# Performance work log

Hardware: AMD Instinct MI355X
Metric: run time of the kernel (lower is better)

The kernel has to match this reference:

```python
import jax, jax.numpy as jnp
import numpy as np
from jax import lax

B, F_BINS, T = 4, 196, 1000
DM, H, DEPTH, FFN, L, EDIM = 512, 8, 64, 2048, 4, 128


def setup_inputs() -> dict:
    key = jax.random.key(0)
    ks = jax.random.split(key, 16)
    d = {}
    d['spec'] = jax.random.normal(ks[0], (B, 1, F_BINS, T), jnp.float32)
    d['conv1_w'] = jax.random.normal(ks[1], (32, 1, 5, 5), jnp.float32) / 5.0
    d['conv1_b'] = jax.random.normal(ks[2], (32,), jnp.float32) * 0.01
    d['conv2_w'] = jax.random.normal(ks[3], (64, 32, 5, 5), jnp.float32) / np.sqrt(32 * 25)
    d['conv2_b'] = jax.random.normal(ks[4], (64,), jnp.float32) * 0.01
    d['proj_w'] = jax.random.normal(ks[5], (DM, 64), jnp.float32) / 8.0
    d['proj_b'] = jnp.zeros((DM,), jnp.float32)
    d['ln1_g'] = jnp.ones((L, DM), jnp.float32)
    d['ln1_b'] = jnp.zeros((L, DM), jnp.float32)
    s = 1.0 / np.sqrt(DM)
    for i, nm in enumerate(['qw', 'kw', 'vw', 'dw']):
        d[nm] = jax.random.normal(ks[6 + i], (L, DM, DM), jnp.float32) * s
    for nm in ['qb', 'kb', 'vb', 'db']:
        d[nm] = jnp.zeros((L, DM), jnp.float32)
    d['Er'] = jax.random.normal(ks[10], (L, T, DEPTH), jnp.float32)
    d['ln2_g'] = jnp.ones((L, DM), jnp.float32)
    d['ln2_b'] = jnp.zeros((L, DM), jnp.float32)
    d['f1w'] = jax.random.normal(ks[11], (L, FFN, DM), jnp.float32) * s
    d['f1b'] = jnp.zeros((L, FFN), jnp.float32)
    d['f2w'] = jax.random.normal(ks[12], (L, DM, FFN), jnp.float32) / np.sqrt(FFN)
    d['f2b'] = jnp.zeros((L, DM), jnp.float32)
    d['deproj_w'] = jax.random.normal(ks[13], (EDIM, DM), jnp.float32) * s
    d['deproj_b'] = jnp.zeros((EDIM,), jnp.float32)
    return d


def _layernorm(x, g, b, eps=1e-5):
    mu = jnp.mean(x, -1, keepdims=True)
    var = jnp.mean(jnp.square(x - mu), -1, keepdims=True)
    return g * (x - mu) / jnp.sqrt(var + eps) + b


def _skew(QEr):
    # QEr: [B,H,S,S] -> music-transformer skew trick
    b, h, s, _ = QEr.shape
    padded = jnp.pad(QEr, ((0, 0), (0, 0), (0, 0), (1, 0)))  # [B,H,S,S+1]
    return padded.reshape(b, h, s + 1, s)[:, :, 1:, :]


def _forward(spec, conv1_w, conv1_b, conv2_w, conv2_b, proj_w, proj_b,
             ln1_g, ln1_b, qw, qb, kw, kb, vw, vb, dw, db, Er,
             ln2_g, ln2_b, f1w, f1b, f2w, f2b, deproj_w, deproj_b):
    dn = ('NCHW', 'OIHW', 'NCHW')
    x = lax.conv_general_dilated(spec, conv1_w, (1, 1), 'SAME', dimension_numbers=dn)
    x = jax.nn.gelu(x + conv1_b[None, :, None, None], approximate=False)
    x = lax.reduce_window(x, -jnp.inf, lax.max, (1, 1, 14, 1), (1, 1, 14, 1), 'VALID')
    x = lax.conv_general_dilated(x, conv2_w, (1, 1), 'SAME', dimension_numbers=dn)
    x = jax.nn.gelu(x + conv2_b[None, :, None, None], approximate=False)
    x = lax.reduce_window(x, -jnp.inf, lax.max, (1, 1, 14, 1), (1, 1, 14, 1), 'VALID')
    x = x.reshape(B, 64, T)              # freq collapsed to 1, flatten(1,2)
    x = x.transpose(0, 2, 1)             # [B,T,64]
    x = x @ proj_w.T + proj_b            # [B,T,DM]
    scale = 1.0 / np.sqrt(DEPTH)
    for l in range(L):
        xn = _layernorm(x, ln1_g[l], ln1_b[l])
        Q = (xn @ qw[l].T + qb[l]).reshape(B, T, H, DEPTH).transpose(0, 2, 1, 3)
        K = (xn @ kw[l].T + kb[l]).reshape(B, T, H, DEPTH).transpose(0, 2, 1, 3)
        V = (xn @ vw[l].T + vb[l]).reshape(B, T, H, DEPTH).transpose(0, 2, 1, 3)
        QEr = jnp.einsum('bhsd,rd->bhsr', Q, Er[l])        # relative pos scores
        Srel = _skew(QEr)
        logits = (jnp.einsum('bhsd,bhtd->bhst', Q, K) + Srel) * scale
        attn = jax.nn.softmax(logits, axis=-1)
        out = jnp.einsum('bhst,bhtd->bhsd', attn, V)
        out = out.transpose(0, 2, 1, 3).reshape(B, T, DM)
        x = x + (out @ dw[l].T + db[l])
        xn2 = _layernorm(x, ln2_g[l], ln2_b[l])
        ff = jax.nn.relu(xn2 @ f1w[l].T + f1b[l]) @ f2w[l].T + f2b[l]
        x = x + ff
    return x @ deproj_w.T + deproj_b     # [B,T,EDIM]


def reference(spec, conv1_w, conv1_b, conv2_w, conv2_b, proj_w, proj_b,
              ln1_g, ln1_b, qw, qb, kw, kb, vw, vb, dw, db, Er,
              ln2_g, ln2_b, f1w, f1b, f2w, f2b, deproj_w, deproj_b):
    return _forward(spec, conv1_w, conv1_b, conv2_w, conv2_b, proj_w, proj_b,
                    ln1_g, ln1_b, qw, qb, kw, kb, vw, vb, dw, db, Er,
                    ln2_g, ln2_b, f1w, f1b, f2w, f2b, deproj_w, deproj_b)
```

## Files before the change

### kernel.cpp

```cpp
#include <hip/hip_runtime.h>
#include <hip/hip_bf16.h>
#include <hip/hip_fp16.h>
#include <math.h>

#define BB 4
#define FBINS 196
#define TT 1000
#define DM 512
#define HH 8
#define DEPTH 64
#define FFN 2048
#define LL 4
#define EDIM 128
#define BT (BB*TT)
#define PSHIFT 12.0f

typedef __hip_bfloat16 bf16;
typedef __attribute__((ext_vector_type(8))) short short8;
typedef __attribute__((ext_vector_type(4))) float floatx4;

#define ARENA_BYTES 420000000ULL
static void* g_arena = nullptr;
__attribute__((constructor)) static void arena_init() {
    if (!g_arena) (void)hipMalloc(&g_arena, ARENA_BYTES);
}

__device__ __forceinline__ float gelu_f(float x) {
    return 0.5f * x * (1.0f + erff(x * 0.70710678118654752440f));
}

__global__ __launch_bounds__(256) void sniff_k(const unsigned short* __restrict__ p,
                                               int n, int* __restrict__ cnt) {
    int i = blockIdx.x * 256 + threadIdx.x;
    int c = 0;
    for (; i < n; i += gridDim.x * 256) {
        unsigned short u = p[i];
        if ((unsigned short)(u & 0x7FFF) > (unsigned short)0x7F80) c++;
    }
    if (c) atomicAdd(cnt, c);
}

#define NCVT 17
struct CvtArgs {
    const void* src[NCVT];
    unsigned dst[NCVT];
    unsigned cum[NCVT + 1];
    const int* cnt;
    float* dstA;
};
__global__ __launch_bounds__(256) void cvt_all(CvtArgs a) {
    unsigned i = blockIdx.x * 256 + threadIdx.x;
    if (i >= a.cum[NCVT]) return;
    bool isb = (*a.cnt == 0);
    int w = 0;
    while (i >= a.cum[w + 1]) w++;
    unsigned j = i - a.cum[w];
    float v = isb ? __bfloat162float(((const bf16*)a.src[w])[j])
                  : ((const float*)a.src[w])[j];
    a.dstA[a.dst[w] + j] = v;
}

__global__ __launch_bounds__(256) void f2bf_dyn(const void* __restrict__ src,
                                                bf16* __restrict__ d, int n,
                                                const int* __restrict__ cnt) {
    int i = blockIdx.x * 256 + threadIdx.x;
    if (i >= n) return;
    if (*cnt == 0) d[i] = ((const bf16*)src)[i];
    else           d[i] = __float2bfloat16(((const float*)src)[i]);
}

__global__ __launch_bounds__(256) void w2perm(const void* __restrict__ src,
                                              bf16* __restrict__ d,
                                              const int* __restrict__ cnt) {
    int idx = blockIdx.x * 256 + threadIdx.x;
    if (idx >= 51200) return;
    int c = idx / 800, k = idx - c * 800;
    int kc = k >> 5, ci = k & 31;
    int di = kc / 5, dj = kc - di * 5;
    int s = ((c * 32 + ci) * 5 + di) * 5 + dj;
    float v = (*cnt == 0) ? __bfloat162float(((const bf16*)src)[s])
                          : ((const float*)src)[s];
    d[idx] = __float2bfloat16(v);
}

__global__ __launch_bounds__(256) void conv1_pool2(const float* __restrict__ spec,
                                                   const float* __restrict__ w1,
                                                   const float* __restrict__ b1,
                                                   bf16* __restrict__ P1c) {
    __shared__ float ss[18][256];
    __shared__ float sw[200];
    int jt = blockIdx.x, p = blockIdx.y, z = blockIdx.z;
    int b = z >> 2, cg = z & 3;
    int tid = threadIdx.x;
    for (int i = tid; i < 200; i += 256) sw[i] = w1[cg * 200 + i];
    int ibase = p * 14, c0 = jt * 250 - 2;
    for (int idx = tid; idx < 18 * 256; idx += 256) {
        int rr = idx >> 8, cc = idx & 255;
        int gi = ibase - 2 + rr, gj = c0 + cc;
        ss[rr][cc] = (gi >= 0 && gi < FBINS && gj >= 0 && gj < TT && cc < 254)
                         ? spec[(size_t)b * FBINS * TT + (size_t)gi * TT + gj] : 0.f;
    }
    __syncthreads();
    if (tid >= 250) return;
    int j = jt * 250 + tid;
    unsigned short* orow = (unsigned short*)P1c + ((size_t)((b * 14 + p) * 1000 + j)) * 32;
    for (int cpl = 0; cpl < 8; cpl += 2) {
        int cp = cg * 8 + cpl;
        float conv[2][14];
        float b0 = b1[cp], b1v = b1[cp + 1];
#pragma unroll
        for (int i = 0; i < 14; i++) { conv[0][i] = b0; conv[1][i] = b1v; }
        const float* w0 = sw + cpl * 25;
        const float* w1p = sw + (cpl + 1) * 25;
        for (int rr = 0; rr < 18; rr++) {
            float v0 = ss[rr][tid], v1 = ss[rr][tid + 1], v2 = ss[rr][tid + 2],
                  v3 = ss[rr][tid + 3], v4 = ss[rr][tid + 4];
#pragma unroll
            for (int di = 0; di < 5; di++) {
                int i = rr - di;
                if (i >= 0 && i < 14) {
                    conv[0][i] += v0 * w0[di * 5] + v1 * w0[di * 5 + 1] + v2 * w0[di * 5 + 2]
                                + v3 * w0[di * 5 + 3] + v4 * w0[di * 5 + 4];
                    conv[1][i] += v0 * w1p[di * 5] + v1 * w1p[di * 5 + 1] + v2 * w1p[di * 5 + 2]
                                + v3 * w1p[di * 5 + 3] + v4 * w1p[di * 5 + 4];
                }
            }
        }
        float m0 = -1e30f, m1 = -1e30f;
#pragma unroll
        for (int i = 0; i < 14; i++) {
            m0 = fmaxf(m0, gelu_f(conv[0][i]));
            m1 = fmaxf(m1, gelu_f(conv[1][i]));
        }
        bf16 mb0 = __float2bfloat16(m0), mb1 = __float2bfloat16(m1);
        unsigned pk = ((unsigned)(*(unsigned short*)&mb1) << 16) |
                      (unsigned)(*(unsigned short*)&mb0);
        *(unsigned*)(orow + cp) = pk;
    }
}

__global__ __launch_bounds__(256) void conv2_gemm(const bf16* __restrict__ P1c,
                                                  const bf16* __restrict__ W2p,
                                                  const float* __restrict__ c2b,
                                                  bf16* __restrict__ convout) {
    __shared__ __align__(16) short Asm[64 * 40];
    __shared__ __align__(16) short Bsm[64 * 40];
    int tid = threadIdx.x, wave = tid >> 6, lane = tid & 63;
    int q = lane >> 4, l15 = lane & 15;
    int jt = blockIdx.x, i = blockIdx.y, b = blockIdx.z;
    int lrow = tid >> 2, lci = (tid & 3) * 8;
    int jrow = jt * 64 + lrow;
    int mw = (wave & 1) * 32, nw = (wave >> 1) * 32;
    floatx4 acc[2][2] = {};
    for (int di = 0; di < 5; di++) {
        int ii = i + di - 2;
        bool iok = (ii >= 0 && ii < 14);
        for (int dj = 0; dj < 5; dj++) {
            int kc = di * 5 + dj;
            {
                int jj = jrow + dj - 2;
                uint4 v = make_uint4(0u, 0u, 0u, 0u);
                if (iok && jrow < TT && jj >= 0 && jj < TT)
                    v = *(const uint4*)(P1c +
                        (((size_t)(b * 14 + ii)) * TT + jj) * 32 + lci);
                *(uint4*)(Asm + lrow * 40 + lci) = v;
            }
            {
                *(uint4*)(Bsm + lrow * 40 + lci) =
                    *(const uint4*)(W2p + (size_t)lrow * 800 + kc * 32 + lci);
            }
            __syncthreads();
            short8 a0 = *(const short8*)(Asm + (mw + l15) * 40 + q * 8);
            short8 a1 = *(const short8*)(Asm + (mw + 16 + l15) * 40 + q * 8);
            short8 b0 = *(const short8*)(Bsm + (nw + l15) * 40 + q * 8);
            short8 b1 = *(const short8*)(Bsm + (nw + 16 + l15) * 40 + q * 8);
            acc[0][0] = __builtin_amdgcn_mfma_f32_16x16x32_bf16(a0, b0, acc[0][0], 0, 0, 0);
            acc[0][1] = __builtin_amdgcn_mfma_f32_16x16x32_bf16(a0, b1, acc[0][1], 0, 0, 0);
            acc[1][0] = __builtin_amdgcn_mfma_f32_16x16x32_bf16(a1, b0, acc[1][0], 0, 0, 0);
            acc[1][1] = __builtin_amdgcn_mfma_f32_16x16x32_bf16(a1, b1, acc[1][1], 0, 0, 0);
            __syncthreads();
        }
    }
#pragma unroll
    for (int im = 0; im < 2; im++) {
#pragma unroll
        for (int jn = 0; jn < 2; jn++) {
            int c = nw + jn * 16 + l15;
            float bv = c2b[c];
#pragma unroll
            for (int r = 0; r < 4; r++) {
                int j = jt * 64 + mw + im * 16 + q * 4 + r;
                if (j >= TT) continue;
                convout[((size_t)(b * 14 + i) * TT + j) * 64 + c] =
                    __float2bfloat16(acc[im][jn][r] + bv);
            }
        }
    }
}

__global__ __launch_bounds__(256) void pool2_k(const bf16* __restrict__ convout,
                                               bf16* __restrict__ p2t) {
    int idx = blockIdx.x * 256 + threadIdx.x;
    if (idx >= 256000) return;
    int c = idx & 63, bj = idx >> 6;
    int b = bj / 1000, j = bj - b * 1000;
    float m = -1e30f;
#pragma unroll
    for (int i = 0; i < 14; i++)
        m = fmaxf(m, gelu_f(__bfloat162float(convout[((size_t)(b * 14 + i) * 1000 + j) * 64 + c])));
    p2t[(size_t)bj * 64 + c] = __float2bfloat16(m);
}

__global__ __launch_bounds__(256) void layernorm_k(const float* __restrict__ x,
                                                   const float* __restrict__ g,
                                                   const float* __restrict__ bta,
                                                   bf16* __restrict__ y) {
    __shared__ float red[256];
    int row = blockIdx.x, tid = threadIdx.x;
    const float* xr = x + (size_t)row * DM;
    float v0 = xr[tid], v1 = xr[tid + 256];
    red[tid] = v0 + v1;
    __syncthreads();
    for (int s = 128; s > 0; s >>= 1) { if (tid < s) red[tid] += red[tid + s]; __syncthreads(); }
    float mu = red[0] * (1.f / 512.f);
    __syncthreads();
    float d0 = v0 - mu, d1 = v1 - mu;
    red[tid] = d0 * d0 + d1 * d1;
    __syncthreads();
    for (int s = 128; s > 0; s >>= 1) { if (tid < s) red[tid] += red[tid + s]; __syncthreads(); }
    float rstd = rsqrtf(red[0] * (1.f / 512.f) + 1e-5f);
    bf16* yr = y + (size_t)row * DM;
    yr[tid]       = __float2bfloat16(d0 * rstd * g[tid]       + bta[tid]);
    yr[tid + 256] = __float2bfloat16(d1 * rstd * g[tid + 256] + bta[tid + 256]);
}

__global__ __launch_bounds__(256) void gemm_out(const float* __restrict__ A,
                                                const float* __restrict__ B,
                                                const float* __restrict__ bias,
                                                const int* __restrict__ cnt,
                                                void* __restrict__ dout,
                                                int M, int N, int K) {
    __shared__ float As[32][33];
    __shared__ float Bs[32][33];
    int tid = threadIdx.x;
    int tx = tid & 15, ty = tid >> 4;
    int m0 = blockIdx.x * 32, n0 = blockIdx.y * 32;
    float c[2][2] = {};
    for (int k0 = 0; k0 < K; k0 += 32) {
#pragma unroll
        for (int i = 0; i < 4; i++) {
            int idx = i * 256 + tid;
            int r = idx >> 5, kk = idx & 31;
            int gm = m0 + r;
            As[r][kk] = (gm < M) ? A[(size_t)gm * K + k0 + kk] : 0.f;
            Bs[r][kk] = B[(size_t)(n0 + r) * K + k0 + kk];
        }
        __syncthreads();
#pragma unroll
        for (int k = 0; k < 32; k++) {
            float a0 = As[ty * 2][k], a1 = As[ty * 2 + 1][k];
            float b0 = Bs[tx * 2][k], b1 = Bs[tx * 2 + 1][k];
            c[0][0] += a0 * b0; c[0][1] += a0 * b1;
            c[1][0] += a1 * b0; c[1][1] += a1 * b1;
        }
        __syncthreads();
    }
    bool isb = (*cnt == 0);
#pragma unroll
    for (int i = 0; i < 2; i++) {
        int m = m0 + ty * 2 + i;
        if (m >= M) continue;
#pragma unroll
        for (int jj = 0; jj < 2; jj++) {
            int n = n0 + tx * 2 + jj;
            float v = c[i][jj] + bias[n];
            if (isb) ((bf16*)dout)[(size_t)m * N + n] = __float2bfloat16(v);
            else     ((float*)dout)[(size_t)m * N + n] = v;
        }
    }
}

template <int BM, int NT, int ROUTE, int ACT, bool OUT_BF16>
__global__ __launch_bounds__(256) void mfma_big(const bf16* __restrict__ A,
                                                const bf16* __restrict__ B,
                                                const float* __restrict__ bias,
                                                const float* __restrict__ resid,
                                                float* __restrict__ Cf,
                                                bf16* __restrict__ Cb,
                                                int M, int N, int K,
                                                size_t wstride, int bstride,
                                                size_t ostride) {
    __shared__ __align__(16) short Asm[BM * 40];
    __shared__ __align__(16) short Bsm[NT * 40];
    int tid = threadIdx.x, wave = tid >> 6, lane = tid & 63;
    int q = lane >> 4, l15 = lane & 15;
    int m0 = blockIdx.x * BM, n0 = blockIdx.y * NT;
    int lrow = tid >> 2, lk = (tid & 3) * 8;
    constexpr int MF = (NT == 128) ? (BM / 16) : (BM / 32);
    int m0w = (NT == 128) ? 0 : ((wave >> 1) * (BM / 2));
    int nfb = (NT == 128) ? (wave * 32) : ((wave & 1) * 32);
    floatx4 acc[MF][2] = {};
    for (int k0 = 0; k0 < K; k0 += 32) {
#pragma unroll
        for (int hh = 0; hh < BM / 64; hh++) {
            int row = lrow + hh * 64, gm = m0 + row;
            uint4 v = make_uint4(0u, 0u, 0u, 0u);
            if (gm < M) v = *(const uint4*)(A + (size_t)gm * K + k0 + lk);
            *(uint4*)(Asm + row * 40 + lk) = v;
        }
#pragma unroll
        for (int hh = 0; hh < NT / 64; hh++) {
            int row = lrow + hh * 64, gn = n0 + row;
            const bf16* src = ROUTE
                ? B + (size_t)(gn >> 9) * wstride + (size_t)(gn & 511) * K + k0 + lk
                : B + (size_t)gn * K + k0 + lk;
            *(uint4*)(Bsm + row * 40 + lk) = *(const uint4*)src;
        }
        __syncthreads();
        short8 a[MF], b2[2];
#pragma unroll
        for (int im = 0; im < MF; im++)
            a[im] = *(const short8*)(Asm + (m0w + im * 16 + l15) * 40 + q * 8);
#pragma unroll
        for (int jn = 0; jn < 2; jn++)
            b2[jn] = *(const short8*)(Bsm + (nfb + jn * 16 + l15) * 40 + q * 8);
#pragma unroll
        for (int im = 0; im < MF; im++)
#pragma unroll
            for (int jn = 0; jn < 2; jn++)
                acc[im][jn] = __builtin_amdgcn_mfma_f32_16x16x32_bf16(
                    a[im], b2[jn], acc[im][jn], 0, 0, 0);
        __syncthreads();
    }
#pragma unroll
    for (int im = 0; im < MF; im++) {
#pragma unroll
        for (int jn = 0; jn < 2; jn++) {
            int nn = n0 + nfb + jn * 16 + l15;
            float bval = ROUTE ? bias[(nn >> 9) * bstride + (nn & 511)] : bias[nn];
#pragma unroll
            for (int r = 0; r < 4; r++) {
                int m = m0 + m0w + im * 16 + q * 4 + r;
                if (m >= M) continue;
                float v = acc[im][jn][r] + bval;
                if (resid) v += resid[(size_t)m * N + nn];
                if (ACT == 1) v = fmaxf(v, 0.f);
                if (ROUTE)
                    Cb[(size_t)(nn >> 9) * ostride + (size_t)m * 512 + (nn & 511)] =
                        __float2bfloat16(v);
                else if (OUT_BF16)
                    Cb[(size_t)m * N + nn] = __float2bfloat16(v);
                else
                    Cf[(size_t)m * N + nn] = v;
            }
        }
    }
}

__global__ __launch_bounds__(256) void vt_k(const bf16* __restrict__ Vb,
                                            bf16* __restrict__ Vt) {
    __shared__ short tile[64][65];
    int t0 = blockIdx.x * 64, z = blockIdx.y;
    int b = z >> 3, h = z & 7;
    int tid = threadIdx.x;
#pragma unroll
    for (int i = 0; i < 16; i++) {
        int tr = i * 4 + (tid >> 6), d = tid & 63;
        int t = t0 + tr;
        bf16 v = (t < TT) ? Vb[((size_t)b * TT + t) * DM + h * 64 + d] : (bf16)__float2bfloat16(0.f);
        tile[tr][d] = *(short*)&v;
    }
    __syncthreads();
#pragma unroll
    for (int i = 0; i < 16; i++) {
        int dr = i * 4 + (tid >> 6), tc = tid & 63;
        *(short*)&Vt[(size_t)z * 65536 + dr * 1024 + t0 + tc] = tile[tc][dr];
    }
}

__global__ __launch_bounds__(256) void score_mfma(const bf16* __restrict__ Q,
                                                  const bf16* __restrict__ K,
                                                  const bf16* __restrict__ Er,
                                                  __half* __restrict__ Sc) {
    __shared__ __align__(16) short SH[16000];
    short* Asm = SH;
    short* Bsm = SH + 3200;
    short* Esm = SH + 8320;
    short* Gl  = SH;
    int tid = threadIdx.x;
    int wave = tid >> 6, lane = tid & 63;
    int q = lane >> 4, l15 = lane & 15;
    int m0 = blockIdx.x * 64, n0 = blockIdx.y * 128;
    int z = blockIdx.z, b = z >> 3, h = z & 7;
    const bf16* Ap = Q + (size_t)b * TT * DM + h * 64;
    const bf16* Bp = K + (size_t)b * TT * DM + h * 64;
    int lrow = tid >> 2, lk = (tid & 3) * 8;
    int db = n0 - m0 - 64;
    floatx4 accS[4][2] = {};
    floatx4 accG[5][3] = {};
    for (int k0 = 0; k0 < 64; k0 += 32) {
        {
            int gm = m0 + lrow;
            uint4 v = make_uint4(0u, 0u, 0u, 0u);
            if (gm < TT) v = *(const uint4*)(Ap + (size_t)gm * DM + k0 + lk);
            *(uint4*)(Asm + lrow * 40 + lk) = v;
            if (tid < 64) {
                int rr = 64 + (tid >> 2);
                int g2 = m0 + rr;
                uint4 v2 = make_uint4(0u, 0u, 0u, 0u);
                if (g2 < TT) v2 = *(const uint4*)(Ap + (size_t)g2 * DM + k0 + lk);
                *(uint4*)(Asm + rr * 40 + lk) = v2;
            }
        }
        {
            int gn = n0 + lrow;
            uint4 v0 = make_uint4(0u, 0u, 0u, 0u), v1 = v0;
            if (gn < TT)      v0 = *(const uint4*)(Bp + (size_t)gn * DM + k0 + lk);
            if (gn + 64 < TT) v1 = *(const uint4*)(Bp + (size_t)(gn + 64) * DM + k0 + lk);
            *(uint4*)(Bsm + lrow * 40 + lk) = v0;
            *(uint4*)(Bsm + (lrow + 64) * 40 + lk) = v1;
        }
        {
#pragma unroll
            for (int hh = 0; hh < 3; hh++) {
                int dd = lrow + hh * 64;
                int dl = db + dd;
                int src = (dl <= 0) ? (999 + dl) : (dl - 1);
                uint4 v = make_uint4(0u, 0u, 0u, 0u);
                if (src >= 0 && src < TT)
                    v = *(const uint4*)(Er + (size_t)src * 64 + k0 + lk);
                *(uint4*)(Esm + dd * 40 + lk) = v;
            }
        }
        __syncthreads();
        short8 a[5], bk[2], e[3];
#pragma unroll
        for (int im = 0; im < 5; im++)
            a[im] = *(const short8*)(Asm + (im * 16 + l15) * 40 + q * 8);
#pragma unroll
        for (int jn = 0; jn < 2; jn++)
            bk[jn] = *(const short8*)(Bsm + (wave * 32 + jn * 16 + l15) * 40 + q * 8);
#pragma unroll
        for (int jg = 0; jg < 3; jg++)
            e[jg] = *(const short8*)(Esm + (wave * 48 + jg * 16 + l15) * 40 + q * 8);
#pragma unroll
        for (int im = 0; im < 4; im++)
#pragma unroll
            for (int jn = 0; jn < 2; jn++)
                accS[im][jn] = __builtin_amdgcn_mfma_f32_16x16x32_bf16(
                    a[im], bk[jn], accS[im][jn], 0, 0, 0);
#pragma unroll
        for (int im = 0; im < 5; im++)
#pragma unroll
            for (int jg = 0; jg < 3; jg++)
                accG[im][jg] = __builtin_amdgcn_mfma_f32_16x16x32_bf16(
                    a[im], e[jg], accG[im][jg], 0, 0, 0);
        __syncthreads();
    }
#pragma unroll
    for (int im = 0; im < 5; im++)
#pragma unroll
        for (int jg = 0; jg < 3; jg++) {
            int col = wave * 48 + jg * 16 + l15;
#pragma unroll
            for (int r = 0; r < 4; r++) {
                int row = im * 16 + q * 4 + r;
                if (row < 65) {
                    bf16 gv = __float2bfloat16(accG[im][jg][r]);
                    Gl[row * 200 + col] = *(short*)&gv;
                }
            }
        }
    __syncthreads();
    __half* Cz = Sc + (size_t)z * 1024000;
#pragma unroll
    for (int im = 0; im < 4; im++) {
#pragma unroll
        for (int jn = 0; jn < 2; jn++) {
            int n = n0 + wave * 32 + jn * 16 + l15;
            if (n >= TT) continue;
#pragma unroll
            for (int r = 0; r < 4; r++) {
                int m = m0 + im * 16 + q * 4 + r;
                if (m >= TT) continue;
                float rel = 0.f;
                if (n != m + 1) {
                    int u = (n <= m) ? m : (m + 1);
                    int dd = n - u - db;
                    short gs = Gl[(u - m0) * 200 + dd];
                    rel = __bfloat162float(*(bf16*)&gs);
                }
                Cz[(size_t)m * 1024 + n] = __float2half((accS[im][jn][r] + rel) * 0.125f);
            }
        }
    }
}

__global__ __launch_bounds__(512) void pv_mfma(const __half* __restrict__ Sc,
                                               const bf16* __restrict__ Vt,
                                               bf16* __restrict__ AO) {
    __shared__ __align__(16) short Asm[64 * 72];
    __shared__ __align__(16) short Vs[64 * 72];
    __shared__ float rowsum[64];
    __shared__ float Oc[4][16][64];
    int tid = threadIdx.x, wave = tid >> 6, lane = tid & 63;
    int q = lane >> 4, l15 = lane & 15;
    int mw = (wave & 3) * 16, kh = wave >> 2;
    int m0 = blockIdx.x * 64;
    int z = blockIdx.z, b = z >> 3, h = z & 7;
    const __half* Ap = Sc + (size_t)z * 1024000;
    const bf16* Bp = Vt + (size_t)z * 65536;
    int lrow = tid >> 3, c = (tid & 7) * 8;
    int chf = c >> 5, cc = c & 31;
    int gm = m0 + lrow;
    bool rowok = (gm < TT);
    float psum = 0.f;
    floatx4 acc[4] = {};
    for (int kb = 0; kb < 512; kb += 32) {
        int t = kb + chf * 512 + cc;
        {
            __attribute__((aligned(16))) short pv8[8];
            if (rowok && t < TT) {
                uint4 u = *(const uint4*)(Ap + (size_t)gm * 1024 + t);
                const __half2* h2 = (const __half2*)&u;
#pragma unroll
                for (int e = 0; e < 4; e++) {
                    float lo = __expf(__low2float(h2[e]) - PSHIFT);
                    float hi = __expf(__high2float(h2[e]) - PSHIFT);
                    psum += lo + hi;
                    bf16 p0 = __float2bfloat16(lo), p1 = __float2bfloat16(hi);
                    pv8[2 * e] = *(short*)&p0; pv8[2 * e + 1] = *(short*)&p1;
                }
            } else {
#pragma unroll
                for (int e = 0; e < 8; e++) pv8[e] = 0;
            }
            *(uint4*)(Asm + lrow * 72 + c) = *(uint4*)pv8;
        }
        *(uint4*)(Vs + lrow * 72 + c) = *(const uint4*)(Bp + (size_t)lrow * 1024 + t);
        __syncthreads();
        short8 a = *(const short8*)(Asm + (mw + l15) * 72 + kh * 32 + q * 8);
#pragma unroll
        for (int jn = 0; jn < 4; jn++) {
            short8 bv = *(const short8*)(Vs + (jn * 16 + l15) * 72 + kh * 32 + q * 8);
            acc[jn] = __builtin_amdgcn_mfma_f32_16x16x32_bf16(a, bv, acc[jn], 0, 0, 0);
        }
        __syncthreads();
    }
    psum += __shfl_xor(psum, 1, 64);
    psum += __shfl_xor(psum, 2, 64);
    psum += __shfl_xor(psum, 4, 64);
    if ((tid & 7) == 0) rowsum[lrow] = psum;
    if (kh == 1) {
#pragma unroll
        for (int jn = 0; jn < 4; jn++)
#pragma unroll
            for (int r = 0; r < 4; r++)
                Oc[wave & 3][q * 4 + r][jn * 16 + l15] = acc[jn][r];
    }
    __syncthreads();
    if (kh == 0) {
#pragma unroll
        for (int r = 0; r < 4; r++) {
            int lm = mw + q * 4 + r;
            int m = m0 + lm;
            if (m >= TT) continue;
            float inv = 1.f / rowsum[lm];
#pragma unroll
            for (int jn = 0; jn < 4; jn++) {
                float o = acc[jn][r] + Oc[wave & 3][q * 4 + r][jn * 16 + l15];
                AO[((size_t)b * TT + m) * DM + h * 64 + jn * 16 + l15] =
                    __float2bfloat16(o * inv);
            }
        }
    }
}

extern "C" void kernel_launch(void* const* d_in, const int* in_sizes, int n_in,
                              void* d_out, int out_size, void* d_ws, size_t ws_size,
                              hipStream_t stream) {
    if (!g_arena) (void)hipMalloc(&g_arena, ARENA_BYTES);
    float* A = (float*)g_arena;

    static const unsigned off[27] = {
        0, 784000, 784800, 784832, 836032, 836096, 868864, 869376, 871424,
        873472, 1922048, 2970624, 4019200, 5067776, 5069824, 5071872,
        5073920, 5075968, 5331968, 5334016, 5336064, 9530368, 9538560,
        13732864, 13734912, 13800448, 13800576};
    const float* spec  = A + off[0];
    const float* c1w   = A + off[1];
    const float* c1b   = A + off[2];
    const float* c2b   = A + off[4];
    const float* projb = A + off[6];
    const float* ln1g  = A + off[7];
    const float* ln1b  = A + off[8];
    const float* qb    = A + off[13];
    const float* db    = A + off[16];
    const float* ln2g  = A + off[18];
    const float* ln2b  = A + off[19];
    const float* f1b   = A + off[21];
    const float* f2b_  = A + off[23];
    const float* depw  = A + off[24];
    const float* depb  = A + off[25];

    const size_t PA = 13800576;
    float* x    = A + PA;
    float* P1   = x + 2048000;
    float* SM   = P1 + 1792000;
    bf16* P1c     = (bf16*)P1;
    bf16* p2t_b   = (bf16*)SM;
    bf16* projw_b = (bf16*)(SM + 128000);
    bf16* w2p     = (bf16*)(SM + 150000);
    int*   cnt  = (int*)(SM + 256000);
    float* ScF  = SM + 256004;
    __half* Sch = (__half*)ScF;
    float* B0   = ScF + 32000000;
    bf16* wb_qkvd = (bf16*)B0;
    bf16* wb_f1   = (bf16*)(B0 + 2097152);
    bf16* wb_f2   = (bf16*)(B0 + 4194304);
    bf16* Erb     = (bf16*)(B0 + 6291456);
    bf16* xn_b    = (bf16*)(B0 + 6419456);
    bf16* AO_b    = (bf16*)(B0 + 7443456);
    bf16* Qb_b    = (bf16*)(B0 + 8467456);
    bf16* Kb_b    = (bf16*)(B0 + 9491456);
    bf16* Vb_b    = (bf16*)(B0 + 10515456);
    bf16* FFH_b   = (bf16*)(B0 + 11539456);
    bf16* Vt      = (bf16*)(B0 + 15635456);
    bf16* convout = (bf16*)(B0 + 16684032);

    hipMemsetAsync(cnt, 0, sizeof(int), stream);
    sniff_k<<<1024, 256, 0, stream>>>((const unsigned short*)d_in[20], 1000000, cnt);

    static const int cvt_ids[NCVT] = {0, 1, 2, 4, 6, 7, 8, 13, 14, 15, 16,
                                      18, 19, 21, 23, 24, 25};
    CvtArgs ca;
    unsigned cum = 0;
    for (int t = 0; t < NCVT; t++) {
        int w = cvt_ids[t];
        ca.src[t] = d_in[w];
        ca.dst[t] = off[w];
        ca.cum[t] = cum;
        cum += off[w + 1] - off[w];
    }
    ca.cum[NCVT] = cum;
    ca.cnt = cnt; ca.dstA = A;
    cvt_all<<<(cum + 255) / 256, 256, 0, stream>>>(ca);

    for (int t = 0; t < 4; t++)
        f2bf_dyn<<<4096, 256, 0, stream>>>(d_in[9 + t], wb_qkvd + (size_t)t * 1048576,
                                           1048576, cnt);
    f2bf_dyn<<<16384, 256, 0, stream>>>(d_in[20], wb_f1, 4194304, cnt);
    f2bf_dyn<<<16384, 256, 0, stream>>>(d_in[22], wb_f2, 4194304, cnt);
    f2bf_dyn<<<1000,  256, 0, stream>>>(d_in[17], Erb,   256000, cnt);
    f2bf_dyn<<<128,   256, 0, stream>>>(d_in[5],  projw_b, 32768, cnt);
    w2perm<<<200, 256, 0, stream>>>(d_in[3], w2p, cnt);

    conv1_pool2<<<dim3(4, 14, 16), 256, 0, stream>>>(spec, c1w, c1b, P1c);
    conv2_gemm<<<dim3(16, 14, 4), 256, 0, stream>>>(P1c, w2p, c2b, convout);
    pool2_k<<<1000, 256, 0, stream>>>(convout, p2t_b);
    mfma_big<64, 64, 0, 0, false><<<dim3(63, 8), 256, 0, stream>>>(
        p2t_b, projw_b, projb, nullptr, x, nullptr, BT, DM, 64, 0, 0, 0);

    for (int l = 0; l < LL; l++) {
        layernorm_k<<<BT, 256, 0, stream>>>(x, ln1g + l * DM, ln1b + l * DM, xn_b);
        mfma_big<128, 128, 1, 0, true><<<dim3(32, 12), 256, 0, stream>>>(
            xn_b, wb_qkvd + (size_t)l * DM * DM, qb + l * DM, nullptr,
            nullptr, Qb_b, BT, 1536, DM, 1048576, 2048, 2048000);
        vt_k<<<dim3(16, 32), 256, 0, stream>>>(Vb_b, Vt);
        score_mfma<<<dim3(16, 8, 32), 256, 0, stream>>>(
            Qb_b, Kb_b, Erb + (size_t)l * TT * DEPTH, Sch);
        pv_mfma<<<dim3(16, 1, 32), 512, 0, stream>>>(Sch, Vt, AO_b);
        mfma_big<64, 64, 0, 0, false><<<dim3(63, 8), 256, 0, stream>>>(
            AO_b, wb_qkvd + 3 * 1048576 + (size_t)l * DM * DM, db + l * DM, x,
            x, nullptr, BT, DM, DM, 0, 0, 0);
        layernorm_k<<<BT, 256, 0, stream>>>(x, ln2g + l * DM, ln2b + l * DM, xn_b);
        mfma_big<128, 128, 0, 1, true><<<dim3(32, 16), 256, 0, stream>>>(
            xn_b, wb_f1 + (size_t)l * FFN * DM, f1b + l * FFN, nullptr,
            nullptr, FFH_b, BT, FFN, DM, 0, 0, 0);
        mfma_big<64, 64, 0, 0, false><<<dim3(63, 8), 256, 0, stream>>>(
            FFH_b, wb_f2 + (size_t)l * DM * FFN, f2b_ + l * DM, x,
            x, nullptr, BT, DM, FFN, 0, 0, 0);
    }

    gemm_out<<<dim3(125, 4), 256, 0, stream>>>(x, depw, depb, cnt, d_out, BT, EDIM, DM);
}
```

Baseline: 1.169 ms.

## Fuse relative-position score and PV kernels into one flash-style attention kernel

Replaces the separate score kernel (which wrote fp16 logits for all 32 batch-heads to global memory) and the PV kernel with one fused kernel. It loops over key tiles, computes QK and Er scores, applies the skew in shared memory, exponentiates with a fixed shift, and accumulates P·V in registers. This removes the large score buffer round trip through HBM and one launch. The cost is a grid of only 512 blocks with serial key loops, so there is less parallelism. Separately, the pooling steps now apply GELU only to the min and max instead of to every element, which relies on GELU being unimodal (decreasing then increasing).

Measured after the change: 1.089 ms. 6.9% less time.

```diff
diff --git a/kernel.cpp b/kernel.cpp
--- a/kernel.cpp
+++ b/kernel.cpp
@@ -126,12 +126,14 @@
                 }
             }
         }
-        float m0 = -1e30f, m1 = -1e30f;
+        float mx0 = -1e30f, mn0 = 1e30f, mx1 = -1e30f, mn1 = 1e30f;
 #pragma unroll
         for (int i = 0; i < 14; i++) {
-            m0 = fmaxf(m0, gelu_f(conv[0][i]));
-            m1 = fmaxf(m1, gelu_f(conv[1][i]));
-        }
+            mx0 = fmaxf(mx0, conv[0][i]); mn0 = fminf(mn0, conv[0][i]);
+            mx1 = fmaxf(mx1, conv[1][i]); mn1 = fminf(mn1, conv[1][i]);
+        }
+        float m0 = fmaxf(gelu_f(mx0), gelu_f(mn0));
+        float m1 = fmaxf(gelu_f(mx1), gelu_f(mn1));
         bf16 mb0 = __float2bfloat16(m0), mb1 = __float2bfloat16(m1);
         unsigned pk = ((unsigned)(*(unsigned short*)&mb1) << 16) |
                       (unsigned)(*(unsigned short*)&mb0);
@@ -204,11 +206,13 @@
     if (idx >= 256000) return;
     int c = idx & 63, bj = idx >> 6;
     int b = bj / 1000, j = bj - b * 1000;
-    float m = -1e30f;
-#pragma unroll
-    for (int i = 0; i < 14; i++)
-        m = fmaxf(m, gelu_f(__bfloat162float(convout[((size_t)(b * 14 + i) * 1000 + j) * 64 + c])));
-    p2t[(size_t)bj * 64 + c] = __float2bfloat16(m);
+    float mx = -1e30f, mn = 1e30f;
+#pragma unroll
+    for (int i = 0; i < 14; i++) {
+        float v = __bfloat162float(convout[((size_t)(b * 14 + i) * 1000 + j) * 64 + c]);
+        mx = fmaxf(mx, v); mn = fminf(mn, v);
+    }
+    p2t[(size_t)bj * 64 + c] = __float2bfloat16(fmaxf(gelu_f(mx), gelu_f(mn)));
 }
 
 __global__ __launch_bounds__(256) void layernorm_k(const float* __restrict__ x,
@@ -378,201 +382,177 @@
     }
 }
 
-__global__ __launch_bounds__(256) void score_mfma(const bf16* __restrict__ Q,
-                                                  const bf16* __restrict__ K,
-                                                  const bf16* __restrict__ Er,
-                                                  __half* __restrict__ Sc) {
-    __shared__ __align__(16) short SH[16000];
-    short* Asm = SH;
-    short* Bsm = SH + 3200;
-    short* Esm = SH + 8320;
-    short* Gl  = SH;
-    int tid = threadIdx.x;
-    int wave = tid >> 6, lane = tid & 63;
+__global__ __launch_bounds__(256, 2) void attn_fused(const bf16* __restrict__ Q,
+                                                     const bf16* __restrict__ K,
+                                                     const bf16* __restrict__ Er,
+                                                     const bf16* __restrict__ Vt,
+                                                     bf16* __restrict__ AO) {
+    __shared__ __align__(16) short Qs[6400];
+    __shared__ __align__(16) short pool[13000];
+    __shared__ __align__(16) short Pl[64 * 136];
+    __shared__ __align__(16) short Vs[64 * 136];
+    __shared__ float rsw[4][64];
+    int tid = threadIdx.x, wave = tid >> 6, lane = tid & 63;
     int q = lane >> 4, l15 = lane & 15;
-    int m0 = blockIdx.x * 64, n0 = blockIdx.y * 128;
+    int m0 = blockIdx.x * 64;
     int z = blockIdx.z, b = z >> 3, h = z & 7;
     const bf16* Ap = Q + (size_t)b * TT * DM + h * 64;
     const bf16* Bp = K + (size_t)b * TT * DM + h * 64;
+    const bf16* Vp = Vt + (size_t)z * 65536;
     int lrow = tid >> 2, lk = (tid & 3) * 8;
-    int db = n0 - m0 - 64;
-    floatx4 accS[4][2] = {};
-    floatx4 accG[5][3] = {};
-    for (int k0 = 0; k0 < 64; k0 += 32) {
-        {
-            int gm = m0 + lrow;
-            uint4 v = make_uint4(0u, 0u, 0u, 0u);
-            if (gm < TT) v = *(const uint4*)(Ap + (size_t)gm * DM + k0 + lk);
-            *(uint4*)(Asm + lrow * 40 + lk) = v;
-            if (tid < 64) {
-                int rr = 64 + (tid >> 2);
-                int g2 = m0 + rr;
-                uint4 v2 = make_uint4(0u, 0u, 0u, 0u);
-                if (g2 < TT) v2 = *(const uint4*)(Ap + (size_t)g2 * DM + k0 + lk);
-                *(uint4*)(Asm + rr * 40 + lk) = v2;
-            }
-        }
-        {
-            int gn = n0 + lrow;
-            uint4 v0 = make_uint4(0u, 0u, 0u, 0u), v1 = v0;
-            if (gn < TT)      v0 = *(const uint4*)(Bp + (size_t)gn * DM + k0 + lk);
-            if (gn + 64 < TT) v1 = *(const uint4*)(Bp + (size_t)(gn + 64) * DM + k0 + lk);
-            *(uint4*)(Bsm + lrow * 40 + lk) = v0;
-            *(uint4*)(Bsm + (lrow + 64) * 40 + lk) = v1;
-        }
-        {
-#pragma unroll
-            for (int hh = 0; hh < 3; hh++) {
-                int dd = lrow + hh * 64;
-                int dl = db + dd;
-                int src = (dl <= 0) ? (999 + dl) : (dl - 1);
-                uint4 v = make_uint4(0u, 0u, 0u, 0u);
-                if (src >= 0 && src < TT)
-                    v = *(const uint4*)(Er + (size_t)src * 64 + k0 + lk);
-                *(uint4*)(Esm + dd * 40 + lk) = v;
-            }
-        }
+    int mw = wave * 16;
+
+#pragma unroll
+    for (int kh = 0; kh < 2; kh++) {
+        int gm = m0 + lrow;
+        uint4 v = make_uint4(0u, 0u, 0u, 0u);
+        if (gm < TT) v = *(const uint4*)(Ap + (size_t)gm * DM + kh * 32 + lk);
+        *(uint4*)(Qs + kh * 3200 + lrow * 40 + lk) = v;
+        if (tid < 64) {
+            int rr = 64 + (tid >> 2);
+            int g2 = m0 + rr;
+            uint4 v2 = make_uint4(0u, 0u, 0u, 0u);
+            if (g2 < TT) v2 = *(const uint4*)(Ap + (size_t)g2 * DM + kh * 32 + lk);
+            *(uint4*)(Qs + kh * 3200 + rr * 40 + lk) = v2;
+        }
+    }
+
+    float rsum[16];
+#pragma unroll
+    for (int i = 0; i < 16; i++) rsum[i] = 0.f;
+    floatx4 accO[4] = {};
+
+    for (int tc = 0; tc < 8; tc++) {
+        int t0 = tc * 128;
+        int db = t0 - m0 - 64;
+        floatx4 accS[4][2] = {};
+        floatx4 accG[5][3] = {};
+        for (int k0 = 0; k0 < 64; k0 += 32) {
+            {
+                int gn = t0 + lrow;
+                uint4 v0 = make_uint4(0u, 0u, 0u, 0u), v1 = v0;
+                if (gn < TT)      v0 = *(const uint4*)(Bp + (size_t)gn * DM + k0 + lk);
+                if (gn + 64 < TT) v1 = *(const uint4*)(Bp + (size_t)(gn + 64) * DM + k0 + lk);
+                *(uint4*)(pool + lrow * 40 + lk) = v0;
+                *(uint4*)(pool + (lrow + 64) * 40 + lk) = v1;
+            }
+            {
+#pragma unroll
+                for (int hh = 0; hh < 3; hh++) {
+                    int dd = lrow + hh * 64;
+                    int dl = db + dd;
+                    int src = (dl <= 0) ? (999 + dl) : (dl - 1);
+                    uint4 v = make_uint4(0u, 0u, 0u, 0u);
+                    if (src >= 0 && src < TT)
+                        v = *(const uint4*)(Er + (size_t)src * 64 + k0 + lk);
+                    *(uint4*)(pool + 5120 + dd * 40 + lk) = v;
+                }
+            }
+            if (k0 == 0) {
+#pragma unroll
+                for (int e = 0; e < 4; e++) {
+                    int li = tid + e * 256;
+                    int row = li >> 4, cs = (li & 15) * 8;
+                    *(uint4*)(Vs + row * 136 + cs) =
+                        *(const uint4*)(Vp + (size_t)row * 1024 + t0 + cs);
+                }
+            }
+            __syncthreads();
+            short8 a[5], bk[2], e[3];
+#pragma unroll
+            for (int im = 0; im < 5; im++)
+                a[im] = *(const short8*)(Qs + (k0 >> 5) * 3200 + (im * 16 + l15) * 40 + q * 8);
+#pragma unroll
+            for (int jn = 0; jn < 2; jn++)
+                bk[jn] = *(const short8*)(pool + (wave * 32 + jn * 16 + l15) * 40 + q * 8);
+#pragma unroll
+            for (int jg = 0; jg < 3; jg++)
+                e[jg] = *(const short8*)(pool + 5120 + (wave * 48 + jg * 16 + l15) * 40 + q * 8);
+#pragma unroll
+            for (int im = 0; im < 4; im++)
+#pragma unroll
+                for (int jn = 0; jn < 2; jn++)
+                    accS[im][jn] = __builtin_amdgcn_mfma_f32_16x16x32_bf16(
+                        a[im], bk[jn], accS[im][jn], 0, 0, 0);
+#pragma unroll
+            for (int im = 0; im < 5; im++)
+#pragma unroll
+                for (int jg = 0; jg < 3; jg++)
+                    accG[im][jg] = __builtin_amdgcn_mfma_f32_16x16x32_bf16(
+                        a[im], e[jg], accG[im][jg], 0, 0, 0);
+            __syncthreads();
+        }
+#pragma unroll
+        for (int im = 0; im < 5; im++)
+#pragma unroll
+            for (int jg = 0; jg < 3; jg++) {
+                int col = wave * 48 + jg * 16 + l15;
+#pragma unroll
+                for (int r = 0; r < 4; r++) {
+                    int row = im * 16 + q * 4 + r;
+                    if (row < 65) {
+                        bf16 gv = __float2bfloat16(accG[im][jg][r]);
+                        pool[row * 200 + col] = *(short*)&gv;
+                    }
+                }
+            }
         __syncthreads();
-        short8 a[5], bk[2], e[3];
-#pragma unroll
-        for (int im = 0; im < 5; im++)
-            a[im] = *(const short8*)(Asm + (im * 16 + l15) * 40 + q * 8);
-#pragma unroll
-        for (int jn = 0; jn < 2; jn++)
-            bk[jn] = *(const short8*)(Bsm + (wave * 32 + jn * 16 + l15) * 40 + q * 8);
-#pragma unroll
-        for (int jg = 0; jg < 3; jg++)
-            e[jg] = *(const short8*)(Esm + (wave * 48 + jg * 16 + l15) * 40 + q * 8);
 #pragma unroll
         for (int im = 0; im < 4; im++)
 #pragma unroll
-            for (int jn = 0; jn < 2; jn++)
-                accS[im][jn] = __builtin_amdgcn_mfma_f32_16x16x32_bf16(
-                    a[im], bk[jn], accS[im][jn], 0, 0, 0);
-#pragma unroll
-        for (int im = 0; im < 5; im++)
-#pragma unroll
-            for (int jg = 0; jg < 3; jg++)
-                accG[im][jg] = __builtin_amdgcn_mfma_f32_16x16x32_bf16(
-                    a[im], e[jg], accG[im][jg], 0, 0, 0);
+            for (int jn = 0; jn < 2; jn++) {
+                int nl = wave * 32 + jn * 16 + l15;
+                int n = t0 + nl;
+#pragma unroll
+                for (int r = 0; r < 4; r++) {
+                    int ml = im * 16 + q * 4 + r;
+                    int m = m0 + ml;
+                    float pe = 0.f;
+                    if (n < TT) {
+                        float rel = 0.f;
+                        if (n != m + 1) {
+                            int u = (n <= m) ? m : (m + 1);
+                            int dd = n - u - db;
+                            short gs = pool[(u - m0) * 200 + dd];
+                            rel = __bfloat162float(*(bf16*)&gs);
+                        }
+                        pe = __expf((accS[im][jn][r] + rel) * 0.125f - PSHIFT);
+                        rsum[im * 4 + r] += pe;
+                    }
+                    bf16 pb = __float2bfloat16(pe);
+                    Pl[ml * 136 + nl] = *(short*)&pb;
+                }
+            }
         __syncthreads();
-    }
-#pragma unroll
-    for (int im = 0; im < 5; im++)
-#pragma unroll
-        for (int jg = 0; jg < 3; jg++) {
-            int col = wave * 48 + jg * 16 + l15;
-#pragma unroll
-            for (int r = 0; r < 4; r++) {
-                int row = im * 16 + q * 4 + r;
-                if (row < 65) {
-                    bf16 gv = __float2bfloat16(accG[im][jg][r]);
-                    Gl[row * 200 + col] = *(short*)&gv;
-                }
-            }
-        }
+#pragma unroll
+        for (int kc = 0; kc < 4; kc++) {
+            short8 a = *(const short8*)(Pl + (mw + l15) * 136 + kc * 32 + q * 8);
+#pragma unroll
+            for (int jn = 0; jn < 4; jn++) {
+                short8 bv = *(const short8*)(Vs + (jn * 16 + l15) * 136 + kc * 32 + q * 8);
+                accO[jn] = __builtin_amdgcn_mfma_f32_16x16x32_bf16(a, bv, accO[jn], 0, 0, 0);
+            }
+        }
+        __syncthreads();
+    }
+#pragma unroll
+    for (int t = 0; t < 16; t++) {
+        float s = rsum[t];
+        s += __shfl_xor(s, 1, 64); s += __shfl_xor(s, 2, 64);
+        s += __shfl_xor(s, 4, 64); s += __shfl_xor(s, 8, 64);
+        if (l15 == 0) rsw[wave][(t >> 2) * 16 + q * 4 + (t & 3)] = s;
+    }
     __syncthreads();
-    __half* Cz = Sc + (size_t)z * 1024000;
-#pragma unroll
-    for (int im = 0; im < 4; im++) {
-#pragma unroll
-        for (int jn = 0; jn < 2; jn++) {
-            int n = n0 + wave * 32 + jn * 16 + l15;
-            if (n >= TT) continue;
-#pragma unroll
-            for (int r = 0; r < 4; r++) {
-                int m = m0 + im * 16 + q * 4 + r;
-                if (m >= TT) continue;
-                float rel = 0.f;
-                if (n != m + 1) {
-                    int u = (n <= m) ? m : (m + 1);
-                    int dd = n - u - db;
-                    short gs = Gl[(u - m0) * 200 + dd];
-                    rel = __bfloat162float(*(bf16*)&gs);
-                }
-                Cz[(size_t)m * 1024 + n] = __float2half((accS[im][jn][r] + rel) * 0.125f);
-            }
-        }
-    }
-}
-
-__global__ __launch_bounds__(512) void pv_mfma(const __half* __restrict__ Sc,
-                                               const bf16* __restrict__ Vt,
-                                               bf16* __restrict__ AO) {
-    __shared__ __align__(16) short Asm[64 * 72];
-    __shared__ __align__(16) short Vs[64 * 72];
-    __shared__ float rowsum[64];
-    __shared__ float Oc[4][16][64];
-    int tid = threadIdx.x, wave = tid >> 6, lane = tid & 63;
-    int q = lane >> 4, l15 = lane & 15;
-    int mw = (wave & 3) * 16, kh = wave >> 2;
-    int m0 = blockIdx.x * 64;
-    int z = blockIdx.z, b = z >> 3, h = z & 7;
-    const __half* Ap = Sc + (size_t)z * 1024000;
-    const bf16* Bp = Vt + (size_t)z * 65536;
-    int lrow = tid >> 3, c = (tid & 7) * 8;
-    int chf = c >> 5, cc = c & 31;
-    int gm = m0 + lrow;
-    bool rowok = (gm < TT);
-    float psum = 0.f;
-    floatx4 acc[4] = {};
-    for (int kb = 0; kb < 512; kb += 32) {
-        int t = kb + chf * 512 + cc;
-        {
-            __attribute__((aligned(16))) short pv8[8];
-            if (rowok && t < TT) {
-                uint4 u = *(const uint4*)(Ap + (size_t)gm * 1024 + t);
-                const __half2* h2 = (const __half2*)&u;
-#pragma unroll
-                for (int e = 0; e < 4; e++) {
-                    float lo = __expf(__low2float(h2[e]) - PSHIFT);
-                    float hi = __expf(__high2float(h2[e]) - PSHIFT);
-                    psum += lo + hi;
-                    bf16 p0 = __float2bfloat16(lo), p1 = __float2bfloat16(hi);
-                    pv8[2 * e] = *(short*)&p0; pv8[2 * e + 1] = *(short*)&p1;
-                }
-            } else {
-#pragma unroll
-                for (int e = 0; e < 8; e++) pv8[e] = 0;
-            }
-            *(uint4*)(Asm + lrow * 72 + c) = *(uint4*)pv8;
-        }
-        *(uint4*)(Vs + lrow * 72 + c) = *(const uint4*)(Bp + (size_t)lrow * 1024 + t);
-        __syncthreads();
-        short8 a = *(const short8*)(Asm + (mw + l15) * 72 + kh * 32 + q * 8);
-#pragma unroll
-        for (int jn = 0; jn < 4; jn++) {
-            short8 bv = *(const short8*)(Vs + (jn * 16 + l15) * 72 + kh * 32 + q * 8);
-            acc[jn] = __builtin_amdgcn_mfma_f32_16x16x32_bf16(a, bv, acc[jn], 0, 0, 0);
-        }
-        __syncthreads();
-    }
-    psum += __shfl_xor(psum, 1, 64);
-    psum += __shfl_xor(psum, 2, 64);
-    psum += __shfl_xor(psum, 4, 64);
-    if ((tid & 7) == 0) rowsum[lrow] = psum;
-    if (kh == 1) {
+#pragma unroll
+    for (int r = 0; r < 4; r++) {
+        int lm = mw + q * 4 + r;
+        int m = m0 + lm;
+        if (m >= TT) continue;
+        float inv = 1.f / (rsw[0][lm] + rsw[1][lm] + rsw[2][lm] + rsw[3][lm]);
 #pragma unroll
         for (int jn = 0; jn < 4; jn++)
-#pragma unroll
-            for (int r = 0; r < 4; r++)
-                Oc[wave & 3][q * 4 + r][jn * 16 + l15] = acc[jn][r];
-    }
-    __syncthreads();
-    if (kh == 0) {
-#pragma unroll
-        for (int r = 0; r < 4; r++) {
-            int lm = mw + q * 4 + r;
-            int m = m0 + lm;
-            if (m >= TT) continue;
-            float inv = 1.f / rowsum[lm];
-#pragma unroll
-            for (int jn = 0; jn < 4; jn++) {
-                float o = acc[jn][r] + Oc[wave & 3][q * 4 + r][jn * 16 + l15];
-                AO[((size_t)b * TT + m) * DM + h * 64 + jn * 16 + l15] =
-                    __float2bfloat16(o * inv);
-            }
-        }
+            AO[((size_t)b * TT + m) * DM + h * 64 + jn * 16 + l15] =
+                __float2bfloat16(accO[jn][r] * inv);
     }
 }
 
@@ -613,7 +593,6 @@
     bf16* w2p     = (bf16*)(SM + 150000);
     int*   cnt  = (int*)(SM + 256000);
     float* ScF  = SM + 256004;
-    __half* Sch = (__half*)ScF;
     float* B0   = ScF + 32000000;
     bf16* wb_qkvd = (bf16*)B0;
     bf16* wb_f1   = (bf16*)(B0 + 2097152);
@@ -667,9 +646,8 @@
             xn_b, wb_qkvd + (size_t)l * DM * DM, qb + l * DM, nullptr,
             nullptr, Qb_b, BT, 1536, DM, 1048576, 2048, 2048000);
         vt_k<<<dim3(16, 32), 256, 0, stream>>>(Vb_b, Vt);
-        score_mfma<<<dim3(16, 8, 32), 256, 0, stream>>>(
-            Qb_b, Kb_b, Erb + (size_t)l * TT * DEPTH, Sch);
-        pv_mfma<<<dim3(16, 1, 32), 512, 0, stream>>>(Sch, Vt, AO_b);
+        attn_fused<<<dim3(16, 1, 32), 256, 0, stream>>>(
+            Qb_b, Kb_b, Erb + (size_t)l * TT * DEPTH, Vt, AO_b);
         mfma_big<64, 64, 0, 0, false><<<dim3(63, 8), 256, 0, stream>>>(
             AO_b, wb_qkvd + 3 * 1048576 + (size_t)l * DM * DM, db + l * DM, x,
             x, nullptr, BT, DM, DM, 0, 0, 0);
```
